# Optimization experiments

Hardware: AMD Instinct MI355X
Metric: run time of the kernel (lower is better)

## Reference

```python
import jax, jax.numpy as jnp
import numpy as np

B, Q, V, H, U = 4, 256, 2048, 512, 128

def setup_inputs() -> dict:
    key = jax.random.key(0)
    ks = jax.random.split(key, 5)
    return {
        "queries": jax.random.normal(ks[0], (B, Q, H), dtype=jnp.float32),
        "values": jax.random.normal(ks[1], (B, V, H), dtype=jnp.float32),
        "w1": jax.random.normal(ks[2], (H, U), dtype=jnp.float32) / np.sqrt(H),
        "w2": jax.random.normal(ks[3], (H, U), dtype=jnp.float32) / np.sqrt(H),
        "v": jax.random.normal(ks[4], (U,), dtype=jnp.float32) / np.sqrt(U),
    }

def reference(queries, values, w1, w2, v):
    # Project queries and values first (cheap GEMMs), then broadcast-add.
    pq = jnp.einsum("bqh,hu->bqu", queries, w1)          # [B,Q,U]
    pv = jnp.einsum("bvh,hu->bvu", values, w2)           # [B,V,U]
    # added_qv: [B,Q,V,U] -- the large intermediate the original materializes
    scores = jnp.einsum("bqvu,u->bqv", jnp.tanh(pq[:, :, None, :] + pv[:, None, :, :]), v)
    attn = jax.nn.softmax(scores, axis=-1)               # softmax over V (last axis, as tf.nn.softmax)
    return jnp.einsum("bqv,bvh->bqh", attn, values)      # [B,Q,H]
```

## Files before the change

### kernel.cpp

```cpp
#include <hip/hip_runtime.h>

#define BB 4
#define QQ 256
#define VV 2048
#define HH 512
#define UU 128

#define C2E   2.8853900817779268f
#define LOG2E 1.4426950408889634f

__device__ __forceinline__ void fma4(float4& a, float s, const float4& w) {
    a.x = fmaf(s, w.x, a.x);
    a.y = fmaf(s, w.y, a.y);
    a.z = fmaf(s, w.z, a.z);
    a.w = fmaf(s, w.w, a.w);
}
__device__ __forceinline__ float2 rcp2(float2 x) {
    return make_float2(__builtin_amdgcn_rcpf(x.x), __builtin_amdgcn_rcpf(x.y));
}
__device__ __forceinline__ float2 mul2(float2 a, float2 b) { return make_float2(a.x*b.x, a.y*b.y); }
__device__ __forceinline__ float2 muls(float2 a, float s)  { return make_float2(a.x*s, a.y*s); }
__device__ __forceinline__ float2 fma2(float2 a, float2 b, float2 c) {
    return make_float2(fmaf(a.x, b.x, c.x), fmaf(a.y, b.y, c.y));
}
__device__ __forceinline__ float2 fmas(float2 a, float s, float2 c) {
    return make_float2(fmaf(a.x, s, c.x), fmaf(a.y, s, c.y));
}

__global__ __launch_bounds__(256) void proj_kernel(const float* __restrict__ queries,
                                                   const float* __restrict__ values,
                                                   const float* __restrict__ w1,
                                                   const float* __restrict__ w2,
                                                   float* __restrict__ pqI,
                                                   float* __restrict__ pvI,
                                                   float* __restrict__ denom) {
    __shared__ float smem[32 * 36 + 32 * 128];
    float (*As)[36] = (float(*)[36])smem;
    float* Ws = smem + 32 * 36;
    float (*Ls)[36] = (float(*)[36])smem;

    const int bid = blockIdx.x;
    const int tid = threadIdx.x;
    if (bid == 0) *(float4*)&denom[tid * 4] = make_float4(0.f, 0.f, 0.f, 0.f);

    const bool isv = (bid < 256);
    const float* A; const float* W; int b, r0, ROWS; float* Ob;
    if (isv) {
        b = bid >> 6; r0 = (bid & 63) * 32;
        A = values + ((size_t)(b * VV + r0)) * HH;  W = w2;
        Ob = pvI + (size_t)b * UU * VV;  ROWS = VV;
    } else {
        const int q = bid - 256;
        b = q >> 3; r0 = (q & 7) * 32;
        A = queries + ((size_t)(b * QQ + r0)) * HH; W = w1;
        Ob = pqI + (size_t)b * UU * QQ;  ROWS = QQ;
    }

    const int tx = tid & 31;
    const int ty = tid >> 5;
    float4 acc[4];
#pragma unroll
    for (int j = 0; j < 4; j++) acc[j] = make_float4(0.f, 0.f, 0.f, 0.f);

    for (int k0 = 0; k0 < HH; k0 += 32) {
        {
            const int r = tid >> 3, kk4 = (tid & 7) * 4;
            const float4 a = *(const float4*)&A[(size_t)r * HH + k0 + kk4];
            As[kk4 + 0][r] = a.x; As[kk4 + 1][r] = a.y;
            As[kk4 + 2][r] = a.z; As[kk4 + 3][r] = a.w;
        }
#pragma unroll
        for (int t = 0; t < 4; t++) {
            const int f = tid + t * 256;
            const int kk = f >> 5, u4 = (f & 31) * 4;
            *(float4*)&Ws[kk * 128 + u4] = *(const float4*)&W[(size_t)(k0 + kk) * UU + u4];
        }
        __syncthreads();
#pragma unroll
        for (int kk = 0; kk < 32; kk++) {
            const float4 a = *(const float4*)&As[kk][ty * 4];
            const float4 w = *(const float4*)&Ws[kk * 128 + tx * 4];
            fma4(acc[0], a.x, w);
            fma4(acc[1], a.y, w);
            fma4(acc[2], a.z, w);
            fma4(acc[3], a.w, w);
        }
        __syncthreads();
    }
#pragma unroll
    for (int j = 0; j < 4; j++) {
        const float aa[4] = {acc[j].x, acc[j].y, acc[j].z, acc[j].w};
#pragma unroll
        for (int i = 0; i < 4; i++)
            Ls[tx * 4 + i][ty * 4 + j] = __builtin_amdgcn_exp2f(aa[i] * C2E);
    }
    __syncthreads();
#pragma unroll
    for (int t = 0; t < 4; t++) {
        const int idx = tid + t * 256;
        const int g = idx >> 5, r = idx & 31;
        float4 o;
        o.x = Ls[4 * g + 0][r]; o.y = Ls[4 * g + 1][r];
        o.z = Ls[4 * g + 2][r]; o.w = Ls[4 * g + 3][r];
        *(float4*)&Ob[((size_t)g * ROWS + r0 + r) * 4] = o;
    }
}

__global__ __launch_bounds__(512, 6) void fused_kernel(const float* __restrict__ pqI,
                                                       const float* __restrict__ pvI,
                                                       const float* __restrict__ vvec,
                                                       const float* __restrict__ values,
                                                       float* __restrict__ slab,
                                                       float* __restrict__ denom) {
    __shared__ float att[256][16];
    __shared__ float scratch[16][512];
    __shared__ float wred[4][16];
    const int tid = threadIdx.x;
    const int bid = blockIdx.x;
    const int vs = bid & 7, qb = (bid >> 3) & 15, b = bid >> 7;
    const int qbase = qb * 16, vbase = vs * 256;

    const int vloc = tid & 255, uh = tid >> 8;
    const int v = vbase + vloc;

    float vsum = 0.0f;
#pragma unroll
    for (int u4 = 0; u4 < UU; u4 += 4) {
        const float4 t = *(const float4*)&vvec[u4];
        vsum += t.x + t.y + t.z + t.w;
    }

    const float* pv4 = pvI + (size_t)b * UU * VV + (size_t)v * 4;
    const float* pq4 = pqI + (size_t)b * UU * QQ + (size_t)qbase * 4;

    float2 acc[8];
#pragma unroll
    for (int p = 0; p < 8; p++) acc[p] = make_float2(0.f, 0.f);

    const int G0 = uh * 16;
    float4 ev = *(const float4*)&pv4[(size_t)G0 * VV * 4];

    for (int g = 0; g < 16; g++) {
        const int G = G0 + g;
        const float* eqp = &pq4[(size_t)G * QQ * 4];
        float4 evn;
        if (g < 15) evn = *(const float4*)&pv4[(size_t)(G + 1) * VV * 4];
        const float4 wq = *(const float4*)&vvec[G * 4];
        const float w0 = 2.f * wq.x, w1 = 2.f * wq.y;
        const float w2 = 2.f * wq.z, w3 = 2.f * wq.w;
#pragma unroll
        for (int p = 0; p < 8; p++) {
            const float4 e0 = *(const float4*)&eqp[(2 * p) * 4];
            const float4 e1 = *(const float4*)&eqp[(2 * p + 1) * 4];
            const float2 a1 = make_float2(fmaf(e0.x, ev.x, 1.f), fmaf(e1.x, ev.x, 1.f));
            const float2 b1 = make_float2(fmaf(e0.y, ev.y, 1.f), fmaf(e1.y, ev.y, 1.f));
            const float2 c1 = make_float2(fmaf(e0.z, ev.z, 1.f), fmaf(e1.z, ev.z, 1.f));
            const float2 d1 = make_float2(fmaf(e0.w, ev.w, 1.f), fmaf(e1.w, ev.w, 1.f));
            const float2 pab = mul2(a1, b1), pcd = mul2(c1, d1);
            const float2 nab = fmas(a1, w1, muls(b1, w0));
            const float2 ncd = fmas(c1, w3, muls(d1, w2));
            const float2 num = fma2(nab, pcd, mul2(ncd, pab));
            const float2 den = mul2(pab, pcd);
            acc[p] = fma2(num, rcp2(den), acc[p]);
        }
        ev = evn;
    }

    float* cbuf = &scratch[0][0];
    if (uh == 1) {
#pragma unroll
        for (int p = 0; p < 8; p++)
            *(float2*)&cbuf[vloc * 16 + 2 * p] = acc[p];
    }
    __syncthreads();
    if (uh == 0) {
#pragma unroll
        for (int p = 0; p < 8; p++) {
            const float2 hi = *(const float2*)&cbuf[vloc * 16 + 2 * p];
            float2 e;
            e.x = __builtin_amdgcn_exp2f((vsum - (acc[p].x + hi.x)) * LOG2E);
            e.y = __builtin_amdgcn_exp2f((vsum - (acc[p].y + hi.y)) * LOG2E);
            att[vloc][2 * p + 0] = e.x;
            att[vloc][2 * p + 1] = e.y;
            acc[p] = e;
        }
#pragma unroll
        for (int off = 1; off < 64; off <<= 1) {
#pragma unroll
            for (int p = 0; p < 8; p++) {
                acc[p].x += __shfl_xor(acc[p].x, off, 64);
                acc[p].y += __shfl_xor(acc[p].y, off, 64);
            }
        }
        if ((tid & 63) == 0) {
            const int w = tid >> 6;
#pragma unroll
            for (int p = 0; p < 8; p++) {
                wred[w][2 * p + 0] = acc[p].x;
                wred[w][2 * p + 1] = acc[p].y;
            }
        }
    }
    __syncthreads();
    if (tid < 16)
        atomicAdd(&denom[b * QQ + qbase + tid],
                  wred[0][tid] + wred[1][tid] + wred[2][tid] + wred[3][tid]);

    const int hg = tid & 127, sel = tid >> 7;
    const int qh = sel & 1, vh = sel >> 1;
    const int h0 = hg * 4;
    const float* vp = values + ((size_t)(b * VV + vbase + vh * 128)) * HH + h0;

    float4 oacc[8];
#pragma unroll
    for (int j = 0; j < 8; j++) oacc[j] = make_float4(0.f, 0.f, 0.f, 0.f);

#pragma unroll 2
    for (int vv = 0; vv < 128; vv++) {
        const float4 w = *(const float4*)&vp[(size_t)vv * HH];
        const float4 a0 = *(const float4*)&att[vh * 128 + vv][qh * 8 + 0];
        const float4 a1 = *(const float4*)&att[vh * 128 + vv][qh * 8 + 4];
        fma4(oacc[0], a0.x, w); fma4(oacc[1], a0.y, w);
        fma4(oacc[2], a0.z, w); fma4(oacc[3], a0.w, w);
        fma4(oacc[4], a1.x, w); fma4(oacc[5], a1.y, w);
        fma4(oacc[6], a1.z, w); fma4(oacc[7], a1.w, w);
    }

    if (vh == 1) {
#pragma unroll
        for (int j = 0; j < 8; j++) *(float4*)&scratch[qh * 8 + j][h0] = oacc[j];
    }
    __syncthreads();
    if (vh == 0) {
        float* sp = slab + (size_t)vs * (BB * QQ * HH);
#pragma unroll
        for (int j = 0; j < 8; j++) {
            const float4 p4 = *(const float4*)&scratch[qh * 8 + j][h0];
            const int q = qh * 8 + j;
            float4 o;
            o.x = oacc[j].x + p4.x; o.y = oacc[j].y + p4.y;
            o.z = oacc[j].z + p4.z; o.w = oacc[j].w + p4.w;
            *(float4*)&sp[((size_t)(b * QQ + qbase + q)) * HH + h0] = o;
        }
    }
}

__global__ __launch_bounds__(256) void reduce_kernel(const float* __restrict__ slab,
                                                     const float* __restrict__ denom,
                                                     float* __restrict__ out) {
    const int i = blockIdx.x * 256 + threadIdx.x;
    const float r = __builtin_amdgcn_rcpf(denom[i >> 7]);
    const float4* s4 = (const float4*)slab;
    float4 s = s4[i];
#pragma unroll
    for (int k = 1; k < 8; k++) {
        const float4 p = s4[(size_t)k * (BB * QQ * HH / 4) + i];
        s.x += p.x; s.y += p.y; s.z += p.z; s.w += p.w;
    }
    s.x *= r; s.y *= r; s.z *= r; s.w *= r;
    ((float4*)out)[i] = s;
}

extern "C" void kernel_launch(void* const* d_in, const int* in_sizes, int n_in,
                              void* d_out, int out_size, void* d_ws, size_t ws_size,
                              hipStream_t stream) {
    const float* queries = (const float*)d_in[0];
    const float* values  = (const float*)d_in[1];
    const float* w1      = (const float*)d_in[2];
    const float* w2      = (const float*)d_in[3];
    const float* vvec    = (const float*)d_in[4];
    float* out = (float*)d_out;

    float* ws    = (float*)d_ws;
    float* pqI   = ws;
    float* pvI   = pqI + BB * UU * QQ;
    float* denom = pvI + (size_t)BB * UU * VV;
    float* slab  = denom + BB * QQ;

    proj_kernel<<<256 + 32, 256, 0, stream>>>(queries, values, w1, w2, pqI, pvI, denom);
    fused_kernel<<<BB * (QQ / 16) * (VV / 256), 512, 0, stream>>>(pqI, pvI, vvec, values, slab, denom);
    reduce_kernel<<<(BB * QQ * HH) / 4 / 256, 256, 0, stream>>>(slab, denom, out);
}
```

Before: 173.3 us.

## Split V into 16 chunks with 256-thread blocks, drop in-block partial reduction

Halves the V chunk per block to 128 and the block size to 256 threads, doubling the grid and removing the shared-memory scratch used to combine two V halves inside a block. Each block now writes its partial output directly to a slab, so the reduce kernel sums 16 slabs instead of 8. This cuts LDS usage and one barrier, but doubles slab write/read traffic in global memory.

```diff
diff --git a/kernel.cpp b/kernel.cpp
--- a/kernel.cpp
+++ b/kernel.cpp
@@ -106,21 +106,20 @@
     }
 }
 
-__global__ __launch_bounds__(512, 6) void fused_kernel(const float* __restrict__ pqI,
+__global__ __launch_bounds__(256, 4) void fused_kernel(const float* __restrict__ pqI,
                                                        const float* __restrict__ pvI,
                                                        const float* __restrict__ vvec,
                                                        const float* __restrict__ values,
                                                        float* __restrict__ slab,
                                                        float* __restrict__ denom) {
-    __shared__ float att[256][16];
-    __shared__ float scratch[16][512];
-    __shared__ float wred[4][16];
+    __shared__ float att[128][16];
+    __shared__ float wred[2][16];
     const int tid = threadIdx.x;
     const int bid = blockIdx.x;
-    const int vs = bid & 7, qb = (bid >> 3) & 15, b = bid >> 7;
-    const int qbase = qb * 16, vbase = vs * 256;
-
-    const int vloc = tid & 255, uh = tid >> 8;
+    const int vs = bid & 15, qb = (bid >> 4) & 15, b = bid >> 8;
+    const int qbase = qb * 16, vbase = vs * 128;
+
+    const int vloc = tid & 127, uh = tid >> 7;
     const int v = vbase + vloc;
 
     float vsum = 0.0f;
@@ -166,22 +165,20 @@
         ev = evn;
     }
 
-    float* cbuf = &scratch[0][0];
     if (uh == 1) {
 #pragma unroll
         for (int p = 0; p < 8; p++)
-            *(float2*)&cbuf[vloc * 16 + 2 * p] = acc[p];
+            *(float2*)&att[vloc][2 * p] = acc[p];
     }
     __syncthreads();
     if (uh == 0) {
 #pragma unroll
         for (int p = 0; p < 8; p++) {
-            const float2 hi = *(const float2*)&cbuf[vloc * 16 + 2 * p];
+            const float2 hi = *(const float2*)&att[vloc][2 * p];
             float2 e;
             e.x = __builtin_amdgcn_exp2f((vsum - (acc[p].x + hi.x)) * LOG2E);
             e.y = __builtin_amdgcn_exp2f((vsum - (acc[p].y + hi.y)) * LOG2E);
-            att[vloc][2 * p + 0] = e.x;
-            att[vloc][2 * p + 1] = e.y;
+            *(float2*)&att[vloc][2 * p] = e;
             acc[p] = e;
         }
 #pragma unroll
@@ -203,13 +200,11 @@
     }
     __syncthreads();
     if (tid < 16)
-        atomicAdd(&denom[b * QQ + qbase + tid],
-                  wred[0][tid] + wred[1][tid] + wred[2][tid] + wred[3][tid]);
-
-    const int hg = tid & 127, sel = tid >> 7;
-    const int qh = sel & 1, vh = sel >> 1;
+        atomicAdd(&denom[b * QQ + qbase + tid], wred[0][tid] + wred[1][tid]);
+
+    const int hg = tid & 127, qh = tid >> 7;
     const int h0 = hg * 4;
-    const float* vp = values + ((size_t)(b * VV + vbase + vh * 128)) * HH + h0;
+    const float* vp = values + ((size_t)(b * VV + vbase)) * HH + h0;
 
     float4 oacc[8];
 #pragma unroll
@@ -218,30 +213,19 @@
 #pragma unroll 2
     for (int vv = 0; vv < 128; vv++) {
         const float4 w = *(const float4*)&vp[(size_t)vv * HH];
-        const float4 a0 = *(const float4*)&att[vh * 128 + vv][qh * 8 + 0];
-        const float4 a1 = *(const float4*)&att[vh * 128 + vv][qh * 8 + 4];
+        const float4 a0 = *(const float4*)&att[vv][qh * 8 + 0];
+        const float4 a1 = *(const float4*)&att[vv][qh * 8 + 4];
         fma4(oacc[0], a0.x, w); fma4(oacc[1], a0.y, w);
         fma4(oacc[2], a0.z, w); fma4(oacc[3], a0.w, w);
         fma4(oacc[4], a1.x, w); fma4(oacc[5], a1.y, w);
         fma4(oacc[6], a1.z, w); fma4(oacc[7], a1.w, w);
     }
 
-    if (vh == 1) {
-#pragma unroll
-        for (int j = 0; j < 8; j++) *(float4*)&scratch[qh * 8 + j][h0] = oacc[j];
-    }
-    __syncthreads();
-    if (vh == 0) {
-        float* sp = slab + (size_t)vs * (BB * QQ * HH);
-#pragma unroll
-        for (int j = 0; j < 8; j++) {
-            const float4 p4 = *(const float4*)&scratch[qh * 8 + j][h0];
-            const int q = qh * 8 + j;
-            float4 o;
-            o.x = oacc[j].x + p4.x; o.y = oacc[j].y + p4.y;
-            o.z = oacc[j].z + p4.z; o.w = oacc[j].w + p4.w;
-            *(float4*)&sp[((size_t)(b * QQ + qbase + q)) * HH + h0] = o;
-        }
+    float* sp = slab + (size_t)vs * (BB * QQ * HH);
+#pragma unroll
+    for (int j = 0; j < 8; j++) {
+        const int q = qh * 8 + j;
+        *(float4*)&sp[((size_t)(b * QQ + qbase + q)) * HH + h0] = oacc[j];
     }
 }
 
@@ -253,7 +237,7 @@
     const float4* s4 = (const float4*)slab;
     float4 s = s4[i];
 #pragma unroll
-    for (int k = 1; k < 8; k++) {
+    for (int k = 1; k < 16; k++) {
         const float4 p = s4[(size_t)k * (BB * QQ * HH / 4) + i];
         s.x += p.x; s.y += p.y; s.z += p.z; s.w += p.w;
     }
@@ -278,6 +262,6 @@
     float* slab  = denom + BB * QQ;
 
     proj_kernel<<<256 + 32, 256, 0, stream>>>(queries, values, w1, w2, pqI, pvI, denom);
-    fused_kernel<<<BB * (QQ / 16) * (VV / 256), 512, 0, stream>>>(pqI, pvI, vvec, values, slab, denom);
+    fused_kernel<<<BB * (QQ / 16) * (VV / 128), 256, 0, stream>>>(pqI, pvI, vvec, values, slab, denom);
     reduce_kernel<<<(BB * QQ * HH) / 4 / 256, 256, 0, stream>>>(slab, denom, out);
 }
```

Result: no change. 173.9 us (+0.3%).
